# Optimization experiments

Measured on AMD Instinct MI355X. Metric: run time of the kernel, lower is better.

## Reference

```python
import jax, jax.numpy as jnp
import numpy as np

N_NODES = 50000
N_EDGES = 640000
N_F = 128
E_F = 128
U_F = 64
HIDDEN = 256
N_GRAPHS = 64


def setup_inputs() -> dict:
    key = jax.random.key(0)
    ks = jax.random.split(key, 12)
    s = 0.02
    x = jax.random.normal(ks[0], (N_NODES, N_F), dtype=jnp.float32)
    edge_index = jax.random.randint(ks[1], (2, N_EDGES), 0, N_NODES, dtype=jnp.int64)
    edge_attr = jax.random.normal(ks[2], (N_EDGES, E_F), dtype=jnp.float32)
    u = jax.random.normal(ks[3], (N_GRAPHS, U_F), dtype=jnp.float32)
    batch = jnp.sort(jax.random.randint(ks[4], (N_NODES,), 0, N_GRAPHS, dtype=jnp.int64))
    # node_mlp_1: Lin(n_f+e_f, hidden) -> ReLU -> Lin(hidden, hidden)
    W1 = jax.random.normal(ks[5], (N_F + E_F, HIDDEN), dtype=jnp.float32) * s
    b1 = jnp.zeros((HIDDEN,), dtype=jnp.float32)
    W2 = jax.random.normal(ks[6], (HIDDEN, HIDDEN), dtype=jnp.float32) * s
    b2 = jnp.zeros((HIDDEN,), dtype=jnp.float32)
    # node_mlp_2: Lin(n_f+hidden+u_f, hidden) -> ReLU -> Lin(hidden, n_f)
    W3 = jax.random.normal(ks[7], (N_F + HIDDEN + U_F, HIDDEN), dtype=jnp.float32) * s
    b3 = jnp.zeros((HIDDEN,), dtype=jnp.float32)
    W4 = jax.random.normal(ks[8], (HIDDEN, N_F), dtype=jnp.float32) * s
    b4 = jnp.zeros((N_F,), dtype=jnp.float32)
    return {"x": x, "edge_index": edge_index, "edge_attr": edge_attr, "u": u,
            "batch": batch, "W1": W1, "b1": b1, "W2": W2, "b2": b2,
            "W3": W3, "b3": b3, "W4": W4, "b4": b4}


def scatter_mean(src, index, dim_size):
    summed = jax.ops.segment_sum(src, index, num_segments=dim_size)
    counts = jax.ops.segment_sum(jnp.ones((src.shape[0],), dtype=src.dtype), index,
                                 num_segments=dim_size)
    return summed / jnp.maximum(counts, 1.0)[:, None]


def reference(x, edge_index, edge_attr, u, batch, W1, b1, W2, b2, W3, b3, W4, b4):
    row, col = edge_index[0], edge_index[1]
    # edge-wise MLP on [x[row] || edge_attr]  -> [E, hidden]
    h = jnp.concatenate([x[row], edge_attr], axis=1)
    h = jax.nn.relu(h @ W1 + b1) @ W2 + b2
    # aggregate messages to destination nodes (mean)
    agg = scatter_mean(h, col, dim_size=x.shape[0])  # [N, hidden]
    # node-wise MLP on [x || agg || u[batch]]
    z = jnp.concatenate([x, agg, u[batch]], axis=1)
    return jax.nn.relu(z @ W3 + b3) @ W4 + b4  # [N, n_f]
```

## Files before the change

kernel.cpp:

```cpp
#include <hip/hip_runtime.h>

#define NNODES 50000
#define NEDGES 640000
#define NF 128
#define EF 128
#define UF 64
#define HID 256
#define ZK 448
#define NSCANB 196

typedef float floatx4 __attribute__((ext_vector_type(4)));
typedef __bf16 bf16x8 __attribute__((ext_vector_type(8)));

__device__ __forceinline__ unsigned short f2bf(float f) {
    unsigned int u = __float_as_uint(f);
    u += 0x7fffu + ((u >> 16) & 1u);
    return (unsigned short)(u >> 16);
}

__device__ __forceinline__ float bf2f(unsigned short h) {
    return __uint_as_float(((unsigned int)h) << 16);
}

__global__ void kconv_t(const float* __restrict__ w, unsigned short* __restrict__ wt,
                        int K, int N) {
    int i = blockIdx.x * 256 + threadIdx.x;
    if (i >= K * N) return;
    int n = i / K, k = i - n * K;
    wt[i] = f2bf(w[(size_t)k * N + n]);
}

__global__ void kxb(const float* __restrict__ x, unsigned short* __restrict__ xb) {
    int i = blockIdx.x * 256 + threadIdx.x;
    if (i >= NNODES * NF / 4) return;
    float4 v = *(const float4*)(x + (size_t)i * 4);
    unsigned lo = (unsigned)f2bf(v.x) | ((unsigned)f2bf(v.y) << 16);
    unsigned hi = (unsigned)f2bf(v.z) | ((unsigned)f2bf(v.w) << 16);
    *(uint2*)&xb[(size_t)i * 4] = make_uint2(lo, hi);
}

__global__ void kfold_w(const float* __restrict__ W2, const float* __restrict__ W3,
                        unsigned short* __restrict__ W3tp) {
    const int k = blockIdx.x;
    const int n = threadIdx.x;
    float v;
    if (k < NF || k >= NF + HID) {
        v = W3[(size_t)k * HID + n];
    } else {
        const int j = k - NF;
        float s = 0.f;
        for (int c = 0; c < HID; ++c)
            s += W2[(size_t)j * HID + c] * W3[(size_t)(NF + c) * HID + n];
        v = s;
    }
    W3tp[(size_t)n * ZK + k] = f2bf(v);
}

__global__ void kfold_b(const float* __restrict__ b2, const float* __restrict__ b3,
                        const float* __restrict__ W3, float* __restrict__ b3p) {
    const int n = threadIdx.x;
    float s = b3[n];
    for (int c = 0; c < HID; ++c)
        s += b2[c] * W3[(size_t)(NF + c) * HID + n];
    b3p[n] = s;
}

__global__ void kcount(const int* __restrict__ eidx, int* __restrict__ cnt) {
    int i = blockIdx.x * 256 + threadIdx.x;
    if (i < NEDGES) atomicAdd(&cnt[eidx[NEDGES + i]], 1);
}

__global__ void kscan1(const int* __restrict__ cnt, int* __restrict__ excl,
                       int* __restrict__ btot) {
    __shared__ int s[256];
    const int t = threadIdx.x, i = blockIdx.x * 256 + t;
    int v = (i < NNODES) ? cnt[i] : 0;
    s[t] = v;
    __syncthreads();
    for (int off = 1; off < 256; off <<= 1) {
        int add = (t >= off) ? s[t - off] : 0;
        __syncthreads();
        s[t] += add;
        __syncthreads();
    }
    if (i < NNODES) excl[i] = s[t] - v;
    if (t == 255) btot[blockIdx.x] = s[255];
}

__global__ void kscan2(int* __restrict__ btot) {
    __shared__ int s[256];
    const int t = threadIdx.x;
    int v = (t < NSCANB) ? btot[t] : 0;
    s[t] = v;
    __syncthreads();
    for (int off = 1; off < 256; off <<= 1) {
        int add = (t >= off) ? s[t - off] : 0;
        __syncthreads();
        s[t] += add;
        __syncthreads();
    }
    if (t < NSCANB) btot[t] = s[t] - v;
}

__global__ void kstart(const int* __restrict__ cnt, const int* __restrict__ excl,
                       const int* __restrict__ btot, int* __restrict__ head,
                       float* __restrict__ inv) {
    int i = blockIdx.x * 256 + threadIdx.x;
    if (i >= NNODES) return;
    head[i] = excl[i] + btot[blockIdx.x];
    int c = cnt[i];
    inv[i] = 1.0f / (float)(c > 1 ? c : 1);
}

__global__ void kscatter(const int* __restrict__ eidx, int* __restrict__ head,
                         int* __restrict__ order, int* __restrict__ sdest) {
    int e = blockIdx.x * 256 + threadIdx.x;
    if (e < NEDGES) {
        int d = eidx[NEDGES + e];
        int p = atomicAdd(&head[d], 1);
        order[p] = e;
        sdest[p] = d;
    }
}

#define ESE2 264

__device__ __forceinline__ int sid(int r) {
    return (((r >> 2) & 3) << 4) + (((r >> 4) & 3) << 2) + (r & 3);
}

__global__ __launch_bounds__(256)
void kscat(const float* __restrict__ ea, const unsigned short* __restrict__ xb,
           const int* __restrict__ eidx, const int* __restrict__ order,
           const int* __restrict__ sdest, const unsigned short* __restrict__ W1t,
           const float* __restrict__ b1, float* __restrict__ agg) {
    __shared__ unsigned short sZ[64 * ESE2];
    __shared__ int sOrd[64], sRow[64], sCol[64];
    const int tid = threadIdx.x;
    const int vb = (blockIdx.x & 7) * 1250 + (blockIdx.x >> 3);
    const int e0 = vb * 64;

    if (tid < 64) {
        int e = order[e0 + tid];
        sOrd[tid] = e;
        sRow[tid] = eidx[e];
        sCol[tid] = sdest[e0 + tid];
    }
    __syncthreads();

    #pragma unroll
    for (int i = 0; i < 4; ++i) {
        int c2 = i * 256 + tid;
        int r = c2 >> 4, ch = c2 & 15;
        uint4 v = *(const uint4*)(xb + (size_t)sRow[sid(r)] * NF + ch * 8);
        *(uint4*)&sZ[r * ESE2 + ch * 8] = v;
    }
    #pragma unroll
    for (int i = 0; i < 8; ++i) {
        int lin = (i << 10) + (tid << 2);
        int r = lin >> 7, c = lin & 127;
        float4 v = *(const float4*)(ea + (size_t)sOrd[sid(r)] * EF + c);
        unsigned lo = (unsigned)f2bf(v.x) | ((unsigned)f2bf(v.y) << 16);
        unsigned hi = (unsigned)f2bf(v.z) | ((unsigned)f2bf(v.w) << 16);
        *(uint2*)&sZ[r * ESE2 + NF + c] = make_uint2(lo, hi);
    }
    __syncthreads();

    const int lane = tid & 63, wave = tid >> 6;
    const int l16 = lane & 15, quad = lane >> 4;
    const int nbase = wave * 64;
    const floatx4 fz = {0.f, 0.f, 0.f, 0.f};

    floatx4 acc[4][4];
    #pragma unroll
    for (int mi = 0; mi < 4; ++mi)
        #pragma unroll
        for (int ni = 0; ni < 4; ++ni) acc[mi][ni] = fz;

    #pragma unroll
    for (int ks = 0; ks < 8; ++ks) {
        const int k0 = ks * 32 + quad * 8;
        bf16x8 a[4], b[4];
        #pragma unroll
        for (int mi = 0; mi < 4; ++mi)
            a[mi] = *(const bf16x8*)&sZ[(mi * 16 + l16) * ESE2 + k0];
        #pragma unroll
        for (int ni = 0; ni < 4; ++ni)
            b[ni] = *(const bf16x8*)&W1t[(size_t)(nbase + ni * 16 + l16) * HID + k0];
        #pragma unroll
        for (int mi = 0; mi < 4; ++mi)
            #pragma unroll
            for (int ni = 0; ni < 4; ++ni)
                acc[mi][ni] = __builtin_amdgcn_mfma_f32_16x16x32_bf16(a[mi], b[ni], acc[mi][ni], 0, 0, 0);
    }

    #pragma unroll
    for (int ni = 0; ni < 4; ++ni) {
        const int n = nbase + ni * 16 + l16;
        const float bias = b1[n];
        const int sbase = quad * 16;
        int d0 = sCol[sbase];
        float s = 0.f;
        #pragma unroll
        for (int mi = 0; mi < 4; ++mi)
            #pragma unroll
            for (int r = 0; r < 4; ++r) {
                const float h = fmaxf(acc[mi][ni][r] + bias, 0.f);
                const int d = sCol[sbase + mi * 4 + r];
                if (d != d0) {
                    unsafeAtomicAdd(&agg[(size_t)d0 * HID + n], s);
                    d0 = d; s = 0.f;
                }
                s += h;
            }
        unsafeAtomicAdd(&agg[(size_t)d0 * HID + n], s);
    }
}

#define ZST 456

__global__ __launch_bounds__(256)
void knode(const float* __restrict__ x, const float* __restrict__ agg,
           const float* __restrict__ inv, const float* __restrict__ u,
           const int* __restrict__ batch,
           const unsigned short* __restrict__ W3t, const float* __restrict__ b3,
           const unsigned short* __restrict__ W4t, const float* __restrict__ b4,
           float* __restrict__ out) {
    __shared__ unsigned short sZ[64 * ZST];
    const int tid = threadIdx.x;
    const int n0 = blockIdx.x * 64;

    {
        const int r = tid >> 2, q = tid & 3;
        const int nc = min(n0 + r, NNODES - 1);
        const float invv = inv[nc];
        const int bg = batch[nc];
        for (int j = 0; j < 28; ++j) {
            const int c = q * 112 + (j << 2);
            float4 v;
            if (c < NF) {
                v = *(const float4*)(x + (size_t)nc * NF + c);
            } else if (c < NF + HID) {
                v = *(const float4*)(agg + (size_t)nc * HID + (c - NF));
                v.x *= invv; v.y *= invv; v.z *= invv; v.w *= invv;
            } else {
                v = *(const float4*)(u + (size_t)bg * UF + (c - NF - HID));
            }
            unsigned lo = (unsigned)f2bf(v.x) | ((unsigned)f2bf(v.y) << 16);
            unsigned hi = (unsigned)f2bf(v.z) | ((unsigned)f2bf(v.w) << 16);
            *(uint2*)&sZ[r * ZST + c] = make_uint2(lo, hi);
        }
    }
    __syncthreads();

    const int lane = tid & 63, wave = tid >> 6;
    const int l16 = lane & 15, quad = lane >> 4;
    const floatx4 fz = {0.f, 0.f, 0.f, 0.f};

    {
        const int nbase = wave * 64;
        floatx4 acc[4][4];
        #pragma unroll
        for (int mi = 0; mi < 4; ++mi)
            #pragma unroll
            for (int ni = 0; ni < 4; ++ni) acc[mi][ni] = fz;

        #pragma unroll 2
        for (int ks = 0; ks < 14; ++ks) {
            const int k0 = ks * 32 + quad * 8;
            bf16x8 a[4], b[4];
            #pragma unroll
            for (int mi = 0; mi < 4; ++mi)
                a[mi] = *(const bf16x8*)&sZ[(mi * 16 + l16) * ZST + k0];
            #pragma unroll
            for (int ni = 0; ni < 4; ++ni)
                b[ni] = *(const bf16x8*)&W3t[(size_t)(nbase + ni * 16 + l16) * ZK + k0];
            #pragma unroll
            for (int mi = 0; mi < 4; ++mi)
                #pragma unroll
                for (int ni = 0; ni < 4; ++ni)
                    acc[mi][ni] = __builtin_amdgcn_mfma_f32_16x16x32_bf16(a[mi], b[ni], acc[mi][ni], 0, 0, 0);
        }
        __syncthreads();
        #pragma unroll
        for (int ni = 0; ni < 4; ++ni) {
            const int n = nbase + ni * 16 + l16;
            const float bias = b3[n];
            #pragma unroll
            for (int mi = 0; mi < 4; ++mi)
                #pragma unroll
                for (int r = 0; r < 4; ++r) {
                    const int row = mi * 16 + quad * 4 + r;
                    sZ[row * ZST + n] = f2bf(fmaxf(acc[mi][ni][r] + bias, 0.f));
                }
        }
        __syncthreads();
    }

    {
        const int nbase = wave * 32;
        floatx4 acc[4][2];
        #pragma unroll
        for (int mi = 0; mi < 4; ++mi)
            #pragma unroll
            for (int ni = 0; ni < 2; ++ni) acc[mi][ni] = fz;

        #pragma unroll 2
        for (int ks = 0; ks < 8; ++ks) {
            const int k0 = ks * 32 + quad * 8;
            bf16x8 a[4], b[2];
            #pragma unroll
            for (int mi = 0; mi < 4; ++mi)
                a[mi] = *(const bf16x8*)&sZ[(mi * 16 + l16) * ZST + k0];
            #pragma unroll
            for (int ni = 0; ni < 2; ++ni)
                b[ni] = *(const bf16x8*)&W4t[(size_t)(nbase + ni * 16 + l16) * HID + k0];
            #pragma unroll
            for (int mi = 0; mi < 4; ++mi)
                #pragma unroll
                for (int ni = 0; ni < 2; ++ni)
                    acc[mi][ni] = __builtin_amdgcn_mfma_f32_16x16x32_bf16(a[mi], b[ni], acc[mi][ni], 0, 0, 0);
        }
        #pragma unroll
        for (int ni = 0; ni < 2; ++ni) {
            const int feat = nbase + ni * 16 + l16;
            const float bias = b4[feat];
            #pragma unroll
            for (int mi = 0; mi < 4; ++mi)
                #pragma unroll
                for (int r = 0; r < 4; ++r) {
                    const int row = mi * 16 + quad * 4 + r;
                    const int n = n0 + row;
                    if (n < NNODES)
                        out[(size_t)n * NF + feat] = acc[mi][ni][r] + bias;
                }
        }
    }
}

extern "C" void kernel_launch(void* const* d_in, const int* in_sizes, int n_in,
                              void* d_out, int out_size, void* d_ws, size_t ws_size,
                              hipStream_t stream) {
    const float* x   = (const float*)d_in[0];
    const int*   ei  = (const int*)d_in[1];
    const float* ea  = (const float*)d_in[2];
    const float* u   = (const float*)d_in[3];
    const int*   bat = (const int*)d_in[4];
    const float* W1  = (const float*)d_in[5];
    const float* b1  = (const float*)d_in[6];
    const float* W2  = (const float*)d_in[7];
    const float* b2  = (const float*)d_in[8];
    const float* W3  = (const float*)d_in[9];
    const float* b3  = (const float*)d_in[10];
    const float* W4  = (const float*)d_in[11];
    const float* b4  = (const float*)d_in[12];
    float* out = (float*)d_out;

    char* p = (char*)d_ws;
    float* agg = (float*)p;                   p += (size_t)NNODES * HID * 4;
    int* cnt   = (int*)p;                     p += (size_t)NNODES * 4;
    float* inv = (float*)p;                   p += (size_t)NNODES * 4;
    int* excl  = (int*)p;                     p += (size_t)NNODES * 4;
    int* btot  = (int*)p;                     p += 256 * 4;
    int* head  = (int*)p;                     p += (size_t)NNODES * 4;
    int* order = (int*)p;                     p += (size_t)NEDGES * 4;
    int* sdest = (int*)p;                     p += (size_t)NEDGES * 4;
    unsigned short* xb  = (unsigned short*)p; p += (size_t)NNODES * NF * 2;
    unsigned short* W1t = (unsigned short*)p; p += (size_t)HID * HID * 2;
    unsigned short* W3tp= (unsigned short*)p; p += (size_t)ZK * HID * 2;
    unsigned short* W4t = (unsigned short*)p; p += (size_t)HID * NF * 2;
    float* b3p = (float*)p;                   p += (size_t)HID * 4;

    hipMemsetAsync(agg, 0, (size_t)NNODES * HID * 4, stream);
    hipMemsetAsync(cnt, 0, (size_t)NNODES * 4, stream);

    kconv_t<<<(HID * HID + 255) / 256, 256, 0, stream>>>(W1, W1t, HID, HID);
    kconv_t<<<(HID * NF + 255) / 256, 256, 0, stream>>>(W4, W4t, HID, NF);
    kxb<<<(NNODES * NF / 4 + 255) / 256, 256, 0, stream>>>(x, xb);
    kfold_w<<<ZK, 256, 0, stream>>>(W2, W3, W3tp);
    kfold_b<<<1, 256, 0, stream>>>(b2, b3, W3, b3p);

    kcount<<<(NEDGES + 255) / 256, 256, 0, stream>>>(ei, cnt);
    kscan1<<<NSCANB, 256, 0, stream>>>(cnt, excl, btot);
    kscan2<<<1, 256, 0, stream>>>(btot);
    kstart<<<NSCANB, 256, 0, stream>>>(cnt, excl, btot, head, inv);
    kscatter<<<(NEDGES + 255) / 256, 256, 0, stream>>>(ei, head, order, sdest);

    kscat<<<NEDGES / 64, 256, 0, stream>>>(ea, xb, ei, order, sdest, W1t, b1, agg);
    knode<<<(NNODES + 63) / 64, 256, 0, stream>>>(x, agg, inv, u, bat, W3tp, b3p, W4t, b4, out);
}
```

Baseline: 887.7 us.

## Enlarge edge tile to 128 rows with 512 threads and pack order/dest

The edge-MLP scatter kernel now processes 128 sorted edges per block with 8 waves, each wave computing a 128x32 output slice, so each W1 fragment loaded from global is reused across twice as many rows. The order and destination arrays are merged into one uint2 array to halve the index loads, and the tile moves to dynamic shared memory (about 69KB per block). Longer destination runs per block may also cut the number of atomic adds into agg. In exchange, shared memory per block and per-wave accumulator register pressure both rise, which may lower occupancy.

```diff
diff --git a/kernel.cpp b/kernel.cpp
--- a/kernel.cpp
+++ b/kernel.cpp
@@ -113,53 +113,57 @@
 }
 
 __global__ void kscatter(const int* __restrict__ eidx, int* __restrict__ head,
-                         int* __restrict__ order, int* __restrict__ sdest) {
+                         uint2* __restrict__ osd) {
     int e = blockIdx.x * 256 + threadIdx.x;
     if (e < NEDGES) {
         int d = eidx[NEDGES + e];
         int p = atomicAdd(&head[d], 1);
-        order[p] = e;
-        sdest[p] = d;
+        osd[p] = make_uint2((unsigned)e, (unsigned)d);
     }
 }
 
 #define ESE2 264
-
-__device__ __forceinline__ int sid(int r) {
-    return (((r >> 2) & 3) << 4) + (((r >> 4) & 3) << 2) + (r & 3);
-}
-
-__global__ __launch_bounds__(256)
+#define SZ_BYTES (128 * ESE2 * 2)
+#define SMEM_BYTES (SZ_BYTES + 3 * 128 * 4)
+
+__device__ __forceinline__ int sid128(int r) {
+    return (((r >> 2) & 3) << 5) + ((r >> 4) << 2) + (r & 3);
+}
+
+__global__ __launch_bounds__(512, 4)
 void kscat(const float* __restrict__ ea, const unsigned short* __restrict__ xb,
-           const int* __restrict__ eidx, const int* __restrict__ order,
-           const int* __restrict__ sdest, const unsigned short* __restrict__ W1t,
+           const int* __restrict__ eidx, const uint2* __restrict__ osd,
+           const unsigned short* __restrict__ W1t,
            const float* __restrict__ b1, float* __restrict__ agg) {
-    __shared__ unsigned short sZ[64 * ESE2];
-    __shared__ int sOrd[64], sRow[64], sCol[64];
+    extern __shared__ char smem[];
+    unsigned short* sZ = (unsigned short*)smem;
+    int* sRow = (int*)(smem + SZ_BYTES);
+    int* sCol = (int*)(smem + SZ_BYTES + 512);
+    int* sOrd = (int*)(smem + SZ_BYTES + 1024);
     const int tid = threadIdx.x;
-    const int vb = (blockIdx.x & 7) * 1250 + (blockIdx.x >> 3);
-    const int e0 = vb * 64;
-
-    if (tid < 64) {
-        int e = order[e0 + tid];
-        sOrd[tid] = e;
-        sRow[tid] = eidx[e];
-        sCol[tid] = sdest[e0 + tid];
+    const int vb = (blockIdx.x & 7) * 625 + (blockIdx.x >> 3);
+    const int e0 = vb * 128;
+
+    if (tid < 128) {
+        uint2 od = osd[e0 + tid];
+        sOrd[tid] = (int)od.x;
+        sCol[tid] = (int)od.y;
+        sRow[tid] = eidx[od.x];
     }
     __syncthreads();
 
     #pragma unroll
     for (int i = 0; i < 4; ++i) {
-        int c2 = i * 256 + tid;
+        int c2 = i * 512 + tid;
         int r = c2 >> 4, ch = c2 & 15;
-        uint4 v = *(const uint4*)(xb + (size_t)sRow[sid(r)] * NF + ch * 8);
+        uint4 v = *(const uint4*)(xb + (size_t)sRow[sid128(r)] * NF + ch * 8);
         *(uint4*)&sZ[r * ESE2 + ch * 8] = v;
     }
     #pragma unroll
     for (int i = 0; i < 8; ++i) {
-        int lin = (i << 10) + (tid << 2);
+        int lin = (i << 11) + (tid << 2);
         int r = lin >> 7, c = lin & 127;
-        float4 v = *(const float4*)(ea + (size_t)sOrd[sid(r)] * EF + c);
+        float4 v = *(const float4*)(ea + (size_t)sOrd[sid128(r)] * EF + c);
         unsigned lo = (unsigned)f2bf(v.x) | ((unsigned)f2bf(v.y) << 16);
         unsigned hi = (unsigned)f2bf(v.z) | ((unsigned)f2bf(v.w) << 16);
         *(uint2*)&sZ[r * ESE2 + NF + c] = make_uint2(lo, hi);
@@ -168,41 +172,38 @@
 
     const int lane = tid & 63, wave = tid >> 6;
     const int l16 = lane & 15, quad = lane >> 4;
-    const int nbase = wave * 64;
+    const int nbase = wave * 32;
     const floatx4 fz = {0.f, 0.f, 0.f, 0.f};
 
-    floatx4 acc[4][4];
-    #pragma unroll
-    for (int mi = 0; mi < 4; ++mi)
-        #pragma unroll
-        for (int ni = 0; ni < 4; ++ni) acc[mi][ni] = fz;
+    floatx4 acc[8][2];
+    #pragma unroll
+    for (int mi = 0; mi < 8; ++mi) {
+        acc[mi][0] = fz;
+        acc[mi][1] = fz;
+    }
 
     #pragma unroll
     for (int ks = 0; ks < 8; ++ks) {
         const int k0 = ks * 32 + quad * 8;
-        bf16x8 a[4], b[4];
-        #pragma unroll
-        for (int mi = 0; mi < 4; ++mi)
-            a[mi] = *(const bf16x8*)&sZ[(mi * 16 + l16) * ESE2 + k0];
-        #pragma unroll
-        for (int ni = 0; ni < 4; ++ni)
-            b[ni] = *(const bf16x8*)&W1t[(size_t)(nbase + ni * 16 + l16) * HID + k0];
-        #pragma unroll
-        for (int mi = 0; mi < 4; ++mi)
-            #pragma unroll
-            for (int ni = 0; ni < 4; ++ni)
-                acc[mi][ni] = __builtin_amdgcn_mfma_f32_16x16x32_bf16(a[mi], b[ni], acc[mi][ni], 0, 0, 0);
-    }
-
-    #pragma unroll
-    for (int ni = 0; ni < 4; ++ni) {
+        bf16x8 b0 = *(const bf16x8*)&W1t[(size_t)(nbase + l16) * HID + k0];
+        bf16x8 b1v = *(const bf16x8*)&W1t[(size_t)(nbase + 16 + l16) * HID + k0];
+        #pragma unroll
+        for (int mi = 0; mi < 8; ++mi) {
+            bf16x8 a = *(const bf16x8*)&sZ[(mi * 16 + l16) * ESE2 + k0];
+            acc[mi][0] = __builtin_amdgcn_mfma_f32_16x16x32_bf16(a, b0, acc[mi][0], 0, 0, 0);
+            acc[mi][1] = __builtin_amdgcn_mfma_f32_16x16x32_bf16(a, b1v, acc[mi][1], 0, 0, 0);
+        }
+    }
+
+    #pragma unroll
+    for (int ni = 0; ni < 2; ++ni) {
         const int n = nbase + ni * 16 + l16;
         const float bias = b1[n];
-        const int sbase = quad * 16;
+        const int sbase = quad * 32;
         int d0 = sCol[sbase];
         float s = 0.f;
         #pragma unroll
-        for (int mi = 0; mi < 4; ++mi)
+        for (int mi = 0; mi < 8; ++mi)
             #pragma unroll
             for (int r = 0; r < 4; ++r) {
                 const float h = fmaxf(acc[mi][ni][r] + bias, 0.f);
@@ -363,8 +364,7 @@
     int* excl  = (int*)p;                     p += (size_t)NNODES * 4;
     int* btot  = (int*)p;                     p += 256 * 4;
     int* head  = (int*)p;                     p += (size_t)NNODES * 4;
-    int* order = (int*)p;                     p += (size_t)NEDGES * 4;
-    int* sdest = (int*)p;                     p += (size_t)NEDGES * 4;
+    uint2* osd = (uint2*)p;                   p += (size_t)NEDGES * 8;
     unsigned short* xb  = (unsigned short*)p; p += (size_t)NNODES * NF * 2;
     unsigned short* W1t = (unsigned short*)p; p += (size_t)HID * HID * 2;
     unsigned short* W3tp= (unsigned short*)p; p += (size_t)ZK * HID * 2;
@@ -384,8 +384,14 @@
     kscan1<<<NSCANB, 256, 0, stream>>>(cnt, excl, btot);
     kscan2<<<1, 256, 0, stream>>>(btot);
     kstart<<<NSCANB, 256, 0, stream>>>(cnt, excl, btot, head, inv);
-    kscatter<<<(NEDGES + 255) / 256, 256, 0, stream>>>(ei, head, order, sdest);
-
-    kscat<<<NEDGES / 64, 256, 0, stream>>>(ea, xb, ei, order, sdest, W1t, b1, agg);
+    kscatter<<<(NEDGES + 255) / 256, 256, 0, stream>>>(ei, head, osd);
+
+    static bool attr_set = false;
+    if (!attr_set) {
+        hipFuncSetAttribute((const void*)kscat,
+                            hipFuncAttributeMaxDynamicSharedMemorySize, SMEM_BYTES);
+        attr_set = true;
+    }
+    kscat<<<NEDGES / 128, 512, SMEM_BYTES, stream>>>(ea, xb, ei, osd, W1t, b1, agg);
     knode<<<(NNODES + 63) / 64, 256, 0, stream>>>(x, agg, inv, u, bat, W3tp, b3p, W4t, b4, out);
 }
```

New measurement: 794.6 us. -10.5%, faster.
